# Performance work log

Hardware: AMD Instinct MI355X
Metric: run time of the kernel (lower is better)

## Reference

```python
import jax, jax.numpy as jnp
import numpy as np

B, S, D, H = 2, 2048, 1024, 8
DK = D // H            # 128
TOPK = int(0.25 * S)   # 512, matches int(topk_ratio * attn_scores.shape[-1])


def setup_inputs() -> dict:
    root = jax.random.key(0)
    ks = jax.random.split(root, 11)
    s = 1.0 / np.sqrt(D)  # nn.Linear default init scale
    def lin(kw, kb):
        W = jax.random.uniform(kw, (D, D), jnp.float32, -s, s)
        b = jax.random.uniform(kb, (D,), jnp.float32, -s, s)
        return W, b
    Wq, bq = lin(ks[0], ks[1])
    Wk, bk = lin(ks[2], ks[3])
    Wv, bv = lin(ks[4], ks[5])
    Wo, bo = lin(ks[6], ks[7])
    return {
        "query": jax.random.normal(ks[8], (B, S, D), jnp.float32),
        "key": jax.random.normal(ks[9], (B, S, D), jnp.float32),
        "value": jax.random.normal(ks[10], (B, S, D), jnp.float32),
        "Wq": Wq, "bq": bq, "Wk": Wk, "bk": bk,
        "Wv": Wv, "bv": bv, "Wo": Wo, "bo": bo,
    }


def reference(query, key, value, Wq, bq, Wk, bk, Wv, bv, Wo, bo):
    # Projections + split heads: [B,S,D] -> [B,S,H,DK]
    Q = (query @ Wq + bq).reshape(B, S, H, DK)
    K = (key   @ Wk + bk).reshape(B, S, H, DK)
    V = (value @ Wv + bv).reshape(B, S, H, DK)

    # Full attention scores [B,H,S,S]
    scores = jnp.einsum('nqhd,nkhd->nhqk', Q, K) / np.sqrt(DK).astype(np.float32)

    # Top-k per query row, scatter into a -1e20-filled tensor
    top_val, top_idx = jax.lax.top_k(scores, TOPK)  # [B,H,S,TOPK]
    bi = jnp.arange(B)[:, None, None, None]
    hi = jnp.arange(H)[None, :, None, None]
    qi = jnp.arange(S)[None, None, :, None]
    sparse = jnp.full(scores.shape, -1e20, scores.dtype).at[bi, hi, qi, top_idx].set(top_val)

    weights = jax.nn.softmax(sparse, axis=-1)                      # [B,H,S,S]
    attn = jnp.einsum('nhql,nlhd->nqhd', weights, V).reshape(B, S, D)
    out = attn @ Wo + bo
    return out, weights
```

## Files before the change

kernel.cpp:

```cpp
#include <hip/hip_runtime.h>
#include <hip/hip_bf16.h>
#include <math.h>

namespace {

constexpr int Bb   = 2;
constexpr int Ss   = 2048;
constexpr int Dd   = 1024;
constexpr int Hh   = 8;
constexpr int DKk  = 128;
constexpr int KTOP = 512;
constexpr int BH    = Bb * Hh;
constexpr int MROWS = Bb * Ss;
constexpr float SCALE = 0.08838834764831845f;

typedef __attribute__((ext_vector_type(8))) short short8t;
typedef __attribute__((ext_vector_type(4))) short short4t;
typedef __attribute__((ext_vector_type(4))) float f32x4;

__device__ inline ushort f2bf(float x) {
  const unsigned u = __float_as_uint(x);
  return (ushort)((u + 0x7FFFu + ((u >> 16) & 1u)) >> 16);
}
__device__ inline float bf2f(ushort h) {
  return __uint_as_float(((unsigned)h) << 16);
}
struct HL { short h, l; };
__device__ inline HL split1(float x) {
  HL r;
  const ushort hu = f2bf(x);
  r.h = (short)hu;
  r.l = (short)f2bf(x - bf2f(hu));
  return r;
}

__device__ inline unsigned key_of(float v) {
  const unsigned u = __float_as_uint(v);
  return (u & 0x80000000u) ? ~u : (u | 0x80000000u);
}
__device__ inline float key_to_float(unsigned k) {
  const unsigned u = (k & 0x80000000u) ? (k & 0x7FFFFFFFu) : ~k;
  return __uint_as_float(u);
}

__device__ inline void gload16(const void* g, void* l) {
  __builtin_amdgcn_global_load_lds(
      (const __attribute__((address_space(1))) unsigned int*)g,
      (__attribute__((address_space(3))) unsigned int*)l, 16, 0, 0);
}

__global__ __launch_bounds__(256) void split_inputs(
    const float* __restrict__ query, const float* __restrict__ keyi,
    const float* __restrict__ value,
    ushort* __restrict__ qsh, ushort* __restrict__ qsl,
    ushort* __restrict__ ksh, ushort* __restrict__ ksl,
    ushort* __restrict__ vsb)
{
  const int z = blockIdx.y;
  const size_t i = ((size_t)blockIdx.x * 256 + threadIdx.x) * 8;
  const float* src = (z == 0) ? query : (z == 1) ? keyi : value;
  const float4 v0 = *(const float4*)(src + i);
  const float4 v1 = *(const float4*)(src + i + 4);
  if (z < 2) {
    ushort* oh = (z == 0) ? qsh : ksh;
    ushort* ol = (z == 0) ? qsl : ksl;
    short8t h, lo;
    HL r;
    r = split1(v0.x); h[0] = r.h; lo[0] = r.l;
    r = split1(v0.y); h[1] = r.h; lo[1] = r.l;
    r = split1(v0.z); h[2] = r.h; lo[2] = r.l;
    r = split1(v0.w); h[3] = r.h; lo[3] = r.l;
    r = split1(v1.x); h[4] = r.h; lo[4] = r.l;
    r = split1(v1.y); h[5] = r.h; lo[5] = r.l;
    r = split1(v1.z); h[6] = r.h; lo[6] = r.l;
    r = split1(v1.w); h[7] = r.h; lo[7] = r.l;
    *(short8t*)(oh + i) = h;
    *(short8t*)(ol + i) = lo;
  } else {
    short8t h;
    h[0] = (short)f2bf(v0.x); h[1] = (short)f2bf(v0.y);
    h[2] = (short)f2bf(v0.z); h[3] = (short)f2bf(v0.w);
    h[4] = (short)f2bf(v1.x); h[5] = (short)f2bf(v1.y);
    h[6] = (short)f2bf(v1.z); h[7] = (short)f2bf(v1.w);
    *(short8t*)(vsb + i) = h;
  }
}

__global__ __launch_bounds__(256) void mfma_proj(
    const ushort* __restrict__ qsh, const ushort* __restrict__ qsl,
    const ushort* __restrict__ ksh, const ushort* __restrict__ ksl,
    const ushort* __restrict__ vsb,
    const ushort* __restrict__ WqTh, const ushort* __restrict__ WqTl,
    const ushort* __restrict__ WkTh, const ushort* __restrict__ WkTl,
    const ushort* __restrict__ WvT,
    const float* __restrict__ bq, const float* __restrict__ bk,
    const float* __restrict__ bv,
    ushort* __restrict__ Qh, ushort* __restrict__ Ql,
    ushort* __restrict__ Kh, ushort* __restrict__ Kl,
    ushort* __restrict__ Vt)
{
  __shared__ ushort Ah[128 * 32];
  __shared__ ushort Al[128 * 32];
  __shared__ ushort Bh[128 * 32];
  __shared__ ushort Bl[128 * 32];
  const int t  = threadIdx.x;
  const int z  = blockIdx.z;
  const int m0 = blockIdx.x * 128;
  const int n0 = blockIdx.y * 128;
  const int l  = t & 63, wv = t >> 6;
  const int wr = wv >> 1, wc = wv & 1;
  const int lrow = l & 15, lhi = l >> 4;

  const ushort* Ah_g = (z == 0) ? qsh : (z == 1) ? ksh : vsb;
  const ushort* Al_g = (z == 0) ? qsl : (z == 1) ? ksl : nullptr;
  const ushort* Bth  = (z == 0) ? WqTh : (z == 1) ? WkTh : WvT;
  const ushort* Btl  = (z == 0) ? WqTl : (z == 1) ? WkTl : nullptr;
  const float*  bias = (z == 0) ? bq   : (z == 1) ? bk   : bv;
  const bool    splitTerms = (z < 2);

  f32x4 acc[4][4] = {};

  for (int kt = 0; kt < Dd; kt += 32) {
#pragma unroll
    for (int p = 0; p < 2; ++p) {
      const int baseRow = p * 64 + wv * 16;
      const int row  = baseRow + (l >> 2);
      const int gl   = (l & 3) ^ (row & 3);
      const size_t ao = (size_t)(m0 + row) * Dd + kt + gl * 8;
      const size_t bo = (size_t)(n0 + row) * Dd + kt + gl * 8;
      gload16(Ah_g + ao, &Ah[baseRow * 32]);
      gload16(Bth + bo, &Bh[baseRow * 32]);
      if (splitTerms) {
        gload16(Al_g + ao, &Al[baseRow * 32]);
        gload16(Btl + bo, &Bl[baseRow * 32]);
      }
    }
    __syncthreads();

    short8t ah[4], al[4], bh[4], bl[4];
#pragma unroll
    for (int i = 0; i < 4; ++i) {
      const int row = wr * 64 + i * 16 + lrow;
      const int idx = row * 32 + ((lhi ^ (row & 3)) << 3);
      ah[i] = *(const short8t*)&Ah[idx];
      if (splitTerms) al[i] = *(const short8t*)&Al[idx];
    }
#pragma unroll
    for (int j = 0; j < 4; ++j) {
      const int row = wc * 64 + j * 16 + lrow;
      const int idx = row * 32 + ((lhi ^ (row & 3)) << 3);
      bh[j] = *(const short8t*)&Bh[idx];
      if (splitTerms) bl[j] = *(const short8t*)&Bl[idx];
    }
#pragma unroll
    for (int i = 0; i < 4; ++i)
#pragma unroll
      for (int j = 0; j < 4; ++j) {
        acc[i][j] = __builtin_amdgcn_mfma_f32_16x16x32_bf16(ah[i], bh[j], acc[i][j], 0, 0, 0);
        if (splitTerms) {
          acc[i][j] = __builtin_amdgcn_mfma_f32_16x16x32_bf16(ah[i], bl[j], acc[i][j], 0, 0, 0);
          acc[i][j] = __builtin_amdgcn_mfma_f32_16x16x32_bf16(al[i], bh[j], acc[i][j], 0, 0, 0);
        }
      }
    __syncthreads();
  }

#pragma unroll
  for (int i = 0; i < 4; ++i) {
#pragma unroll
    for (int j = 0; j < 4; ++j) {
      const int nn = n0 + wc * 64 + j * 16 + lrow;
#pragma unroll
      for (int r = 0; r < 4; ++r) {
        const int mm = m0 + wr * 64 + i * 16 + lhi * 4 + r;
        const float v = acc[i][j][r] + bias[nn];
        const int bb = mm >> 11, s = mm & (Ss - 1);
        const int hh = nn >> 7,  dk = nn & (DKk - 1);
        if (z < 2) {
          const size_t o = (((size_t)(bb * Hh + hh)) * Ss + s) * DKk + dk;
          const HL rr = split1(v);
          if (z == 0) { Qh[o] = (ushort)rr.h; Ql[o] = (ushort)rr.l; }
          else        { Kh[o] = (ushort)rr.h; Kl[o] = (ushort)rr.l; }
        } else {
          Vt[((size_t)((bb * Hh + hh) * DKk + dk)) * Ss + s] = f2bf(v);
        }
      }
    }
  }
}

__global__ __launch_bounds__(256) void mfma_scores(
    const ushort* __restrict__ Qh, const ushort* __restrict__ Ql,
    const ushort* __restrict__ Kh, const ushort* __restrict__ Kl,
    unsigned* __restrict__ wtsOut)
{
  __shared__ ushort Ah[128 * 32];
  __shared__ ushort Al[128 * 32];
  __shared__ ushort Bh[128 * 32];
  __shared__ ushort Bl[128 * 32];
  const int t  = threadIdx.x;
  const int z  = blockIdx.z;
  const int n0 = blockIdx.x * 128;
  const int m0 = blockIdx.y * 128;
  const int l  = t & 63, wv = t >> 6;
  const int wr = wv >> 1, wc = wv & 1;
  const int lrow = l & 15, lhi = l >> 4;
  const size_t boff = (size_t)z * Ss * DKk;

  f32x4 acc[4][4] = {};

  for (int kt = 0; kt < DKk; kt += 32) {
#pragma unroll
    for (int p = 0; p < 2; ++p) {
      const int baseRow = p * 64 + wv * 16;
      const int row  = baseRow + (l >> 2);
      const int gl   = (l & 3) ^ (row & 3);
      const size_t ao = boff + (size_t)(m0 + row) * DKk + kt + gl * 8;
      const size_t bo = boff + (size_t)(n0 + row) * DKk + kt + gl * 8;
      gload16(Qh + ao, &Ah[baseRow * 32]);
      gload16(Ql + ao, &Al[baseRow * 32]);
      gload16(Kh + bo, &Bh[baseRow * 32]);
      gload16(Kl + bo, &Bl[baseRow * 32]);
    }
    __syncthreads();

    short8t ah[4], al[4], bh[4], bl[4];
#pragma unroll
    for (int i = 0; i < 4; ++i) {
      const int row = wr * 64 + i * 16 + lrow;
      const int idx = row * 32 + ((lhi ^ (row & 3)) << 3);
      ah[i] = *(const short8t*)&Ah[idx];
      al[i] = *(const short8t*)&Al[idx];
    }
#pragma unroll
    for (int j = 0; j < 4; ++j) {
      const int row = wc * 64 + j * 16 + lrow;
      const int idx = row * 32 + ((lhi ^ (row & 3)) << 3);
      bh[j] = *(const short8t*)&Bh[idx];
      bl[j] = *(const short8t*)&Bl[idx];
    }
#pragma unroll
    for (int i = 0; i < 4; ++i)
#pragma unroll
      for (int j = 0; j < 4; ++j) {
        acc[i][j] = __builtin_amdgcn_mfma_f32_16x16x32_bf16(ah[i], bh[j], acc[i][j], 0, 0, 0);
        acc[i][j] = __builtin_amdgcn_mfma_f32_16x16x32_bf16(ah[i], bl[j], acc[i][j], 0, 0, 0);
        acc[i][j] = __builtin_amdgcn_mfma_f32_16x16x32_bf16(al[i], bh[j], acc[i][j], 0, 0, 0);
      }
    __syncthreads();
  }

#pragma unroll
  for (int i = 0; i < 4; ++i)
#pragma unroll
    for (int j = 0; j < 4; ++j) {
      const int nn = n0 + wc * 64 + j * 16 + lrow;
#pragma unroll
      for (int r = 0; r < 4; ++r) {
        const int mm = m0 + wr * 64 + i * 16 + lhi * 4 + r;
        wtsOut[(size_t)z * Ss * Ss + (size_t)mm * Ss + nn] =
            key_of(acc[i][j][r] * SCALE);
      }
    }
}

__global__ __launch_bounds__(256) void mfma_oproj(
    const float* __restrict__ pv0, const float* __restrict__ pv1,
    const ushort* __restrict__ Bt,
    const float* __restrict__ bias, float* __restrict__ Cout)
{
  __shared__ ushort As[128 * 64];
  __shared__ ushort Bs[128 * 64];
  const int t  = threadIdx.x;
  const int m0 = blockIdx.x * 128;
  const int n0 = blockIdx.y * 128;
  const int l  = t & 63, wv = t >> 6;
  const int wr = wv >> 1, wc = wv & 1;
  const int lrow = l & 15, lhi = l >> 4;

  f32x4 acc[4][4] = {};

  for (int kt = 0; kt < Dd; kt += 64) {
#pragma unroll
    for (int p = 0; p < 4; ++p) {
      const int baseRow = p * 32 + wv * 8;
      const int brow = baseRow + (l >> 3);
      const int bgl  = (l & 7) ^ (brow & 7);
      gload16(Bt + (size_t)(n0 + brow) * Dd + kt + bgl * 8, &Bs[baseRow * 64]);
      const int li = p * 256 + t, row = li >> 3, g = li & 7;
      const int sw = row * 64 + ((g ^ (row & 7)) << 3);
      const size_t ao = (size_t)(m0 + row) * Dd + kt + g * 8;
      const float4 a0 = *(const float4*)(pv0 + ao);
      const float4 a1 = *(const float4*)(pv0 + ao + 4);
      const float4 c0 = *(const float4*)(pv1 + ao);
      const float4 c1 = *(const float4*)(pv1 + ao + 4);
      short8t sa;
      sa[0] = (short)f2bf(a0.x + c0.x); sa[1] = (short)f2bf(a0.y + c0.y);
      sa[2] = (short)f2bf(a0.z + c0.z); sa[3] = (short)f2bf(a0.w + c0.w);
      sa[4] = (short)f2bf(a1.x + c1.x); sa[5] = (short)f2bf(a1.y + c1.y);
      sa[6] = (short)f2bf(a1.z + c1.z); sa[7] = (short)f2bf(a1.w + c1.w);
      *(short8t*)&As[sw] = sa;
    }
    __syncthreads();

#pragma unroll
    for (int kk = 0; kk < 2; ++kk) {
      short8t a[4], b[4];
      const int g = kk * 4 + lhi;
#pragma unroll
      for (int i = 0; i < 4; ++i) {
        const int row = wr * 64 + i * 16 + lrow;
        a[i] = *(const short8t*)&As[row * 64 + ((g ^ (row & 7)) << 3)];
      }
#pragma unroll
      for (int j = 0; j < 4; ++j) {
        const int row = wc * 64 + j * 16 + lrow;
        b[j] = *(const short8t*)&Bs[row * 64 + ((g ^ (row & 7)) << 3)];
      }
#pragma unroll
      for (int i = 0; i < 4; ++i)
#pragma unroll
        for (int j = 0; j < 4; ++j)
          acc[i][j] = __builtin_amdgcn_mfma_f32_16x16x32_bf16(a[i], b[j], acc[i][j], 0, 0, 0);
    }
    __syncthreads();
  }

#pragma unroll
  for (int i = 0; i < 4; ++i)
#pragma unroll
    for (int j = 0; j < 4; ++j) {
      const int nn = n0 + wc * 64 + j * 16 + lrow;
#pragma unroll
      for (int r = 0; r < 4; ++r) {
        const int mm = m0 + wr * 64 + i * 16 + lhi * 4 + r;
        Cout[(size_t)mm * Dd + nn] = acc[i][j][r] + bias[nn];
      }
    }
}

__global__ __launch_bounds__(256) void pv_split(
    const float* __restrict__ Wts, const ushort* __restrict__ VtAll,
    float* __restrict__ pvp)
{
  __shared__ ushort As[128 * 64];
  __shared__ ushort Bs[128 * 64];
  const int t  = threadIdx.x;
  const int ks = blockIdx.x;
  const int m0 = blockIdx.y * 128;
  const int z  = blockIdx.z;
  const int l  = t & 63, wv = t >> 6;
  const int wr = wv >> 1, wc = wv & 1;
  const int lrow = l & 15, lhi = l >> 4;

  const float*  Af = Wts + (size_t)z * Ss * Ss;
  const ushort* Bt = VtAll + (size_t)z * DKk * Ss;

  f32x4 acc[4][4] = {};

  for (int kt = ks * 1024; kt < ks * 1024 + 1024; kt += 64) {
#pragma unroll
    for (int p = 0; p < 4; ++p) {
      const int baseRow = p * 32 + wv * 8;
      const int brow = baseRow + (l >> 3);
      const int bgl  = (l & 7) ^ (brow & 7);
      gload16(Bt + (size_t)brow * Ss + kt + bgl * 8, &Bs[baseRow * 64]);
      const int li = p * 256 + t, row = li >> 3, g = li & 7;
      const int sw = row * 64 + ((g ^ (row & 7)) << 3);
      const float* src = Af + (size_t)(m0 + row) * Ss + kt + g * 8;
      const float4 v0 = *(const float4*)src;
      const float4 v1 = *(const float4*)(src + 4);
      short8t sa;
      sa[0] = (short)f2bf(v0.x); sa[1] = (short)f2bf(v0.y);
      sa[2] = (short)f2bf(v0.z); sa[3] = (short)f2bf(v0.w);
      sa[4] = (short)f2bf(v1.x); sa[5] = (short)f2bf(v1.y);
      sa[6] = (short)f2bf(v1.z); sa[7] = (short)f2bf(v1.w);
      *(short8t*)&As[sw] = sa;
    }
    __syncthreads();

#pragma unroll
    for (int kk = 0; kk < 2; ++kk) {
      short8t a[4], b[4];
      const int g = kk * 4 + lhi;
#pragma unroll
      for (int i = 0; i < 4; ++i) {
        const int row = wr * 64 + i * 16 + lrow;
        a[i] = *(const short8t*)&As[row * 64 + ((g ^ (row & 7)) << 3)];
      }
#pragma unroll
      for (int j = 0; j < 4; ++j) {
        const int row = wc * 64 + j * 16 + lrow;
        b[j] = *(const short8t*)&Bs[row * 64 + ((g ^ (row & 7)) << 3)];
      }
#pragma unroll
      for (int i = 0; i < 4; ++i)
#pragma unroll
        for (int j = 0; j < 4; ++j)
          acc[i][j] = __builtin_amdgcn_mfma_f32_16x16x32_bf16(a[i], b[j], acc[i][j], 0, 0, 0);
    }
    __syncthreads();
  }

  const int bb = z >> 3, hh = z & 7;
  float* outp = pvp + (size_t)ks * MROWS * Dd;
#pragma unroll
  for (int i = 0; i < 4; ++i)
#pragma unroll
    for (int j = 0; j < 4; ++j) {
      const int nn = wc * 64 + j * 16 + lrow;
#pragma unroll
      for (int r = 0; r < 4; ++r) {
        const int mm = m0 + wr * 64 + i * 16 + lhi * 4 + r;
        outp[((size_t)(bb * Ss + mm)) * Dd + hh * DKk + nn] = acc[i][j][r];
      }
    }
}

__global__ __launch_bounds__(256) void transpose_bf16(
    const float* __restrict__ W, ushort* __restrict__ Wt)
{
  __shared__ float tile[32][33];
  const int t  = threadIdx.x;
  const int c0 = blockIdx.x * 32, r0 = blockIdx.y * 32;
  const int lr = t >> 3, lc4 = (t & 7) * 4;
  const float4 v = *(const float4*)(W + (size_t)(r0 + lr) * Dd + c0 + lc4);
  tile[lr][lc4 + 0] = v.x; tile[lr][lc4 + 1] = v.y;
  tile[lr][lc4 + 2] = v.z; tile[lr][lc4 + 3] = v.w;
  __syncthreads();
  const int oc = t >> 3, or4 = (t & 7) * 4;
  short4t o;
  o[0] = (short)f2bf(tile[or4 + 0][oc]);
  o[1] = (short)f2bf(tile[or4 + 1][oc]);
  o[2] = (short)f2bf(tile[or4 + 2][oc]);
  o[3] = (short)f2bf(tile[or4 + 3][oc]);
  *(short4t*)(Wt + (size_t)(c0 + oc) * Dd + r0 + or4) = o;
}

__global__ __launch_bounds__(256) void transpose_split(
    const float* __restrict__ W, ushort* __restrict__ Th, ushort* __restrict__ Tl)
{
  __shared__ float tile[32][33];
  const int t  = threadIdx.x;
  const int c0 = blockIdx.x * 32, r0 = blockIdx.y * 32;
  const int lr = t >> 3, lc4 = (t & 7) * 4;
  const float4 v = *(const float4*)(W + (size_t)(r0 + lr) * Dd + c0 + lc4);
  tile[lr][lc4 + 0] = v.x; tile[lr][lc4 + 1] = v.y;
  tile[lr][lc4 + 2] = v.z; tile[lr][lc4 + 3] = v.w;
  __syncthreads();
  const int oc = t >> 3, or4 = (t & 7) * 4;
  short4t oh, ol;
  HL r;
  r = split1(tile[or4 + 0][oc]); oh[0] = r.h; ol[0] = r.l;
  r = split1(tile[or4 + 1][oc]); oh[1] = r.h; ol[1] = r.l;
  r = split1(tile[or4 + 2][oc]); oh[2] = r.h; ol[2] = r.l;
  r = split1(tile[or4 + 3][oc]); oh[3] = r.h; ol[3] = r.l;
  *(short4t*)(Th + (size_t)(c0 + oc) * Dd + r0 + or4) = oh;
  *(short4t*)(Tl + (size_t)(c0 + oc) * Dd + r0 + or4) = ol;
}

__global__ __launch_bounds__(256) void topk_softmax(float* __restrict__ wts)
{
  __shared__ unsigned histAll[4][1088];

  const int lane = threadIdx.x & 63;
  const int wv   = threadIdx.x >> 6;
  const int row  = blockIdx.x * 4 + wv;
  float* rowp = wts + (size_t)row * Ss;
  unsigned* rowu = (unsigned*)rowp;
  unsigned* h = histAll[wv];

  unsigned k[32];
  unsigned lmax = 0u;
#pragma unroll
  for (int i = 0; i < 8; ++i) {
    const uint4 v = *(const uint4*)(rowu + i * 256 + lane * 4);
    k[i * 4 + 0] = v.x; k[i * 4 + 1] = v.y;
    k[i * 4 + 2] = v.z; k[i * 4 + 3] = v.w;
    lmax = max(max(lmax, max(v.x, v.y)), max(v.z, v.w));
  }
#pragma unroll
  for (int off = 32; off > 0; off >>= 1) lmax = max(lmax, __shfl_xor(lmax, off));
  const float m = key_to_float(lmax);

  unsigned needK = KTOP, tieC = 0u, prefix = 0u;

  {
#pragma unroll
    for (int i = 0; i < 17; ++i) h[lane + i * 64] = 0u;
#pragma unroll
    for (int i = 0; i < 32; ++i) {
      const unsigned b = k[i] >> 22;
      atomicAdd(&h[b + (b >> 4)], 1u);
    }
    unsigned b[16], lsum = 0u;
#pragma unroll
    for (int i = 0; i < 16; ++i) { b[i] = h[lane * 17 + i]; lsum += b[i]; }
    unsigned s = lsum;
#pragma unroll
    for (int off = 1; off < 64; off <<= 1) {
      const unsigned v = __shfl_down(s, off);
      if (lane + off < 64) s += v;
    }
    unsigned run = s - lsum;
    unsigned fb = 0u, fn = 0u, ft = 0u;
    bool found = false;
#pragma unroll
    for (int i = 15; i >= 0; --i) {
      const unsigned c = b[i];
      if (!found && c > 0u && run < needK && run + c >= needK) {
        found = true; fb = (unsigned)(lane * 16 + i); fn = needK - run; ft = c;
      }
      run += c;
    }
    const unsigned long long msk = __ballot(found);
    const int src = (int)__ffsll(msk) - 1;
    prefix = __shfl(fb, src) << 22;
    needK  = __shfl(fn, src);
    tieC   = __shfl(ft, src);
  }

#pragma unroll
  for (int pass = 0; pass < 2; ++pass) {
    const int sh = (pass == 0) ? 14 : 6;
    const int ph = sh + 8;
#pragma unroll
    for (int i = 0; i < 5; ++i) h[lane + i * 64] = 0u;
    const unsigned pcmp = prefix >> ph;
#pragma unroll
    for (int i = 0; i < 32; ++i) {
      if ((k[i] >> ph) == pcmp) {
        const unsigned b = (k[i] >> sh) & 255u;
        atomicAdd(&h[b + (b >> 4)], 1u);
      }
    }
    unsigned b4[4], lsum = 0u;
#pragma unroll
    for (int i = 0; i < 4; ++i) {
      const unsigned x = (unsigned)(lane * 4 + i);
      b4[i] = h[x + (x >> 4)];
      lsum += b4[i];
    }
    unsigned s = lsum;
#pragma unroll
    for (int off = 1; off < 64; off <<= 1) {
      const unsigned v = __shfl_down(s, off);
      if (lane + off < 64) s += v;
    }
    unsigned run = s - lsum;
    unsigned fb = 0u, fn = 0u, ft = 0u;
    bool found = false;
#pragma unroll
    for (int i = 3; i >= 0; --i) {
      const unsigned c = b4[i];
      if (!found && c > 0u && run < needK && run + c >= needK) {
        found = true; fb = (unsigned)(lane * 4 + i); fn = needK - run; ft = c;
      }
      run += c;
    }
    const unsigned long long msk = __ballot(found);
    const int src = (int)__ffsll(msk) - 1;
    prefix |= __shfl(fb, src) << sh;
    needK   = __shfl(fn, src);
    tieC    = __shfl(ft, src);
  }

  unsigned T;
  {
    h[lane] = 0u;
    if (lane < 4) h[64 + lane] = 0u;
    const unsigned pcmp = prefix >> 6;
#pragma unroll
    for (int i = 0; i < 32; ++i) {
      if ((k[i] >> 6) == pcmp) {
        const unsigned b = k[i] & 63u;
        atomicAdd(&h[b + (b >> 4)], 1u);
      }
    }
    const unsigned b0 = h[lane + (lane >> 4)];
    unsigned s = b0;
#pragma unroll
    for (int off = 1; off < 64; off <<= 1) {
      const unsigned v = __shfl_down(s, off);
      if (lane + off < 64) s += v;
    }
    const unsigned run = s - b0;
    const bool found = (b0 > 0u && run < needK && run + b0 >= needK);
    const unsigned long long msk = __ballot(found);
    const int src = (int)__ffsll(msk) - 1;
    T     = prefix | (unsigned)__shfl((unsigned)lane, src);
    needK = __shfl(needK - run, src);
    tieC  = __shfl(b0, src);
  }

  if (tieC != needK) {
    unsigned R = 0u;
#pragma unroll
    for (int i = 0; i < 8; ++i) {
      unsigned myEq = 0u;
#pragma unroll
      for (int c = 0; c < 4; ++c) myEq += (k[i * 4 + c] == T);
      unsigned ps = myEq;
#pragma unroll
      for (int off = 1; off < 64; off <<= 1) {
        const unsigned v = __shfl_up(ps, off);
        if (lane >= off) ps += v;
      }
      unsigned before = R + ps - myEq;
#pragma unroll
      for (int c = 0; c < 4; ++c) {
        if (k[i * 4 + c] == T) {
          if (before >= needK) k[i * 4 + c] = 0u;
          ++before;
        }
      }
      R += __shfl(ps, 63);
    }
  }

  float lz = 0.f;
#pragma unroll
  for (int i = 0; i < 32; ++i) {
    const unsigned kk = k[i];
    const float w = (kk >= T) ? __expf(key_to_float(kk) - m) : 0.f;
    k[i] = __float_as_uint(w);
    lz += w;
  }
#pragma unroll
  for (int off = 32; off > 0; off >>= 1) lz += __shfl_xor(lz, off);
  const float Zi = 1.0f / lz;

#pragma unroll
  for (int i = 0; i < 8; ++i) {
    float4 o;
    o.x = __uint_as_float(k[i * 4 + 0]) * Zi;
    o.y = __uint_as_float(k[i * 4 + 1]) * Zi;
    o.z = __uint_as_float(k[i * 4 + 2]) * Zi;
    o.w = __uint_as_float(k[i * 4 + 3]) * Zi;
    *(float4*)(rowu + i * 256 + lane * 4) = o;
  }
}

}

extern "C" void kernel_launch(void* const* d_in, const int* in_sizes, int n_in,
                              void* d_out_v, int out_size, void* d_ws, size_t ws_size,
                              hipStream_t stream)
{
  const float* query = (const float*)d_in[0];
  const float* key   = (const float*)d_in[1];
  const float* value = (const float*)d_in[2];
  const float* Wq = (const float*)d_in[3];  const float* bq = (const float*)d_in[4];
  const float* Wk = (const float*)d_in[5];  const float* bk = (const float*)d_in[6];
  const float* Wv = (const float*)d_in[7];  const float* bv = (const float*)d_in[8];
  const float* Wo = (const float*)d_in[9];  const float* bo = (const float*)d_in[10];

  float* d_out = (float*)d_out_v;
  float* outp  = d_out;
  float* wts   = d_out + (size_t)Bb * Ss * Dd;

  const size_t PROJ = (size_t)MROWS * Dd;
  const size_t DD2  = (size_t)Dd * Dd;

  ushort* ws    = (ushort*)d_ws;
  ushort* Qh    = ws;
  ushort* Ql    = Qh + PROJ;
  ushort* Kh    = Ql + PROJ;
  ushort* Kl    = Kh + PROJ;
  ushort* wreg  = Kl + PROJ;
  ushort* WqTh  = wreg;
  ushort* WqTl  = wreg + DD2;
  ushort* WkTh  = wreg + 2 * DD2;
  ushort* WkTl  = wreg + 3 * DD2;
  ushort* WvT   = wreg + 4 * DD2;
  ushort* WoT   = wreg + 5 * DD2;
  ushort* Vt    = wreg + 6 * DD2;
  float*  pvp   = (float*)Qh;

  ushort* qsh = (ushort*)wts;
  ushort* qsl = qsh + PROJ;
  ushort* ksh = qsh + 2 * PROJ;
  ushort* ksl = qsh + 3 * PROJ;
  ushort* vsb = qsh + 4 * PROJ;

  const dim3 blk(256);

  transpose_split<<<dim3(32, 32), blk, 0, stream>>>(Wq, WqTh, WqTl);
  transpose_split<<<dim3(32, 32), blk, 0, stream>>>(Wk, WkTh, WkTl);
  transpose_bf16<<<dim3(32, 32), blk, 0, stream>>>(Wv, WvT);
  transpose_bf16<<<dim3(32, 32), blk, 0, stream>>>(Wo, WoT);

  split_inputs<<<dim3((int)(PROJ / 2048), 3), blk, 0, stream>>>(
      query, key, value, qsh, qsl, ksh, ksl, vsb);

  mfma_proj<<<dim3(MROWS / 128, Dd / 128, 3), blk, 0, stream>>>(
      qsh, qsl, ksh, ksl, vsb, WqTh, WqTl, WkTh, WkTl, WvT,
      bq, bk, bv, Qh, Ql, Kh, Kl, Vt);

  mfma_scores<<<dim3(Ss / 128, Ss / 128, BH), blk, 0, stream>>>(
      Qh, Ql, Kh, Kl, (unsigned*)wts);

  topk_softmax<<<dim3(BH * Ss / 4), blk, 0, stream>>>(wts);

  pv_split<<<dim3(2, Ss / 128, BH), blk, 0, stream>>>(wts, Vt, pvp);

  mfma_oproj<<<dim3(MROWS / 128, Dd / 128), blk, 0, stream>>>(
      pvp, pvp + (size_t)MROWS * Dd, WoT, bo, outp);
}
```

Before: 387.1 us.

## Fuse top-k softmax with PV matmul and merge weight transposes

Merges the top-k/softmax kernel with the probability-times-V product. Each block handles 16 query rows, normalizes them, then immediately multiplies them against V with MFMA, reducing across four waves in shared memory and writing bf16 attention output. This drops the split-K fp32 partial buffers and the separate re-read of the weights tile. The output projection now loads bf16 directly, and the four weight-transpose launches are combined into one. The risks are that PV now reads A and V straight from global memory without LDS tiling, and that V is re-read by every 16-row block.

```diff
diff --git a/kernel.cpp b/kernel.cpp
--- a/kernel.cpp
+++ b/kernel.cpp
@@ -86,6 +86,47 @@
   }
 }
 
+__global__ __launch_bounds__(256) void transpose_prep(
+    const float* __restrict__ Wq, const float* __restrict__ Wk,
+    const float* __restrict__ Wv, const float* __restrict__ Wo,
+    ushort* __restrict__ WqTh, ushort* __restrict__ WqTl,
+    ushort* __restrict__ WkTh, ushort* __restrict__ WkTl,
+    ushort* __restrict__ WvT,  ushort* __restrict__ WoT)
+{
+  __shared__ float tile[32][33];
+  const int z = blockIdx.z;
+  const float* W = (z == 0) ? Wq : (z == 1) ? Wk : (z == 2) ? Wv : Wo;
+  const int t  = threadIdx.x;
+  const int c0 = blockIdx.x * 32, r0 = blockIdx.y * 32;
+  const int lr = t >> 3, lc4 = (t & 7) * 4;
+  const float4 v = *(const float4*)(W + (size_t)(r0 + lr) * Dd + c0 + lc4);
+  tile[lr][lc4 + 0] = v.x; tile[lr][lc4 + 1] = v.y;
+  tile[lr][lc4 + 2] = v.z; tile[lr][lc4 + 3] = v.w;
+  __syncthreads();
+  const int oc = t >> 3, or4 = (t & 7) * 4;
+  const size_t o = (size_t)(c0 + oc) * Dd + r0 + or4;
+  if (z < 2) {
+    ushort* Th = (z == 0) ? WqTh : WkTh;
+    ushort* Tl = (z == 0) ? WqTl : WkTl;
+    short4t oh, ol;
+    HL r;
+    r = split1(tile[or4 + 0][oc]); oh[0] = r.h; ol[0] = r.l;
+    r = split1(tile[or4 + 1][oc]); oh[1] = r.h; ol[1] = r.l;
+    r = split1(tile[or4 + 2][oc]); oh[2] = r.h; ol[2] = r.l;
+    r = split1(tile[or4 + 3][oc]); oh[3] = r.h; ol[3] = r.l;
+    *(short4t*)(Th + o) = oh;
+    *(short4t*)(Tl + o) = ol;
+  } else {
+    ushort* Wt = (z == 2) ? WvT : WoT;
+    short4t ov;
+    ov[0] = (short)f2bf(tile[or4 + 0][oc]);
+    ov[1] = (short)f2bf(tile[or4 + 1][oc]);
+    ov[2] = (short)f2bf(tile[or4 + 2][oc]);
+    ov[3] = (short)f2bf(tile[or4 + 3][oc]);
+    *(short4t*)(Wt + o) = ov;
+  }
+}
+
 __global__ __launch_bounds__(256) void mfma_proj(
     const ushort* __restrict__ qsh, const ushort* __restrict__ qsl,
     const ushort* __restrict__ ksh, const ushort* __restrict__ ksl,
@@ -264,9 +305,262 @@
     }
 }
 
+__global__ __launch_bounds__(256) void topk_pv(
+    float* __restrict__ wts, const ushort* __restrict__ VtAll,
+    ushort* __restrict__ attnb)
+{
+  __shared__ unsigned histAll[4][1088];
+  __shared__ float    red[2][16][128];
+
+  const int t    = threadIdx.x;
+  const int lane = t & 63;
+  const int wv   = t >> 6;
+  const int bh   = blockIdx.x >> 7;
+  const int q0   = (blockIdx.x & 127) * 16;
+  unsigned* h = histAll[wv];
+
+  for (int rr = 0; rr < 4; ++rr) {
+    const int row = q0 + wv * 4 + rr;
+    float* rowp = wts + ((size_t)bh * Ss + row) * Ss;
+    unsigned* rowu = (unsigned*)rowp;
+
+    unsigned k[32];
+    unsigned lmax = 0u;
+#pragma unroll
+    for (int i = 0; i < 8; ++i) {
+      const uint4 v = *(const uint4*)(rowu + i * 256 + lane * 4);
+      k[i * 4 + 0] = v.x; k[i * 4 + 1] = v.y;
+      k[i * 4 + 2] = v.z; k[i * 4 + 3] = v.w;
+      lmax = max(max(lmax, max(v.x, v.y)), max(v.z, v.w));
+    }
+#pragma unroll
+    for (int off = 32; off > 0; off >>= 1) lmax = max(lmax, __shfl_xor(lmax, off));
+    const float m = key_to_float(lmax);
+
+    unsigned needK = KTOP, tieC = 0u, prefix = 0u;
+
+    {
+#pragma unroll
+      for (int i = 0; i < 17; ++i) h[lane + i * 64] = 0u;
+#pragma unroll
+      for (int i = 0; i < 32; ++i) {
+        const unsigned b = k[i] >> 22;
+        atomicAdd(&h[b + (b >> 4)], 1u);
+      }
+      unsigned b[16], lsum = 0u;
+#pragma unroll
+      for (int i = 0; i < 16; ++i) { b[i] = h[lane * 17 + i]; lsum += b[i]; }
+      unsigned s = lsum;
+#pragma unroll
+      for (int off = 1; off < 64; off <<= 1) {
+        const unsigned v = __shfl_down(s, off);
+        if (lane + off < 64) s += v;
+      }
+      unsigned run = s - lsum;
+      unsigned fb = 0u, fn = 0u, ft = 0u;
+      bool found = false;
+#pragma unroll
+      for (int i = 15; i >= 0; --i) {
+        const unsigned c = b[i];
+        if (!found && c > 0u && run < needK && run + c >= needK) {
+          found = true; fb = (unsigned)(lane * 16 + i); fn = needK - run; ft = c;
+        }
+        run += c;
+      }
+      const unsigned long long msk = __ballot(found);
+      const int src = (int)__ffsll(msk) - 1;
+      prefix = __shfl(fb, src) << 22;
+      needK  = __shfl(fn, src);
+      tieC   = __shfl(ft, src);
+    }
+
+#pragma unroll
+    for (int pass = 0; pass < 2; ++pass) {
+      const int sh = (pass == 0) ? 14 : 6;
+      const int ph = sh + 8;
+#pragma unroll
+      for (int i = 0; i < 5; ++i) h[lane + i * 64] = 0u;
+      const unsigned pcmp = prefix >> ph;
+#pragma unroll
+      for (int i = 0; i < 32; ++i) {
+        if ((k[i] >> ph) == pcmp) {
+          const unsigned b = (k[i] >> sh) & 255u;
+          atomicAdd(&h[b + (b >> 4)], 1u);
+        }
+      }
+      unsigned b4[4], lsum = 0u;
+#pragma unroll
+      for (int i = 0; i < 4; ++i) {
+        const unsigned x = (unsigned)(lane * 4 + i);
+        b4[i] = h[x + (x >> 4)];
+        lsum += b4[i];
+      }
+      unsigned s = lsum;
+#pragma unroll
+      for (int off = 1; off < 64; off <<= 1) {
+        const unsigned v = __shfl_down(s, off);
+        if (lane + off < 64) s += v;
+      }
+      unsigned run = s - lsum;
+      unsigned fb = 0u, fn = 0u, ft = 0u;
+      bool found = false;
+#pragma unroll
+      for (int i = 3; i >= 0; --i) {
+        const unsigned c = b4[i];
+        if (!found && c > 0u && run < needK && run + c >= needK) {
+          found = true; fb = (unsigned)(lane * 4 + i); fn = needK - run; ft = c;
+        }
+        run += c;
+      }
+      const unsigned long long msk = __ballot(found);
+      const int src = (int)__ffsll(msk) - 1;
+      prefix |= __shfl(fb, src) << sh;
+      needK   = __shfl(fn, src);
+      tieC    = __shfl(ft, src);
+    }
+
+    unsigned T;
+    {
+      h[lane] = 0u;
+      if (lane < 4) h[64 + lane] = 0u;
+      const unsigned pcmp = prefix >> 6;
+#pragma unroll
+      for (int i = 0; i < 32; ++i) {
+        if ((k[i] >> 6) == pcmp) {
+          const unsigned b = k[i] & 63u;
+          atomicAdd(&h[b + (b >> 4)], 1u);
+        }
+      }
+      const unsigned b0 = h[lane + (lane >> 4)];
+      unsigned s = b0;
+#pragma unroll
+      for (int off = 1; off < 64; off <<= 1) {
+        const unsigned v = __shfl_down(s, off);
+        if (lane + off < 64) s += v;
+      }
+      const unsigned run = s - b0;
+      const bool found = (b0 > 0u && run < needK && run + b0 >= needK);
+      const unsigned long long msk = __ballot(found);
+      const int src = (int)__ffsll(msk) - 1;
+      T     = prefix | (unsigned)__shfl((unsigned)lane, src);
+      needK = __shfl(needK - run, src);
+      tieC  = __shfl(b0, src);
+    }
+
+    if (tieC != needK) {
+      unsigned R = 0u;
+#pragma unroll
+      for (int i = 0; i < 8; ++i) {
+        unsigned myEq = 0u;
+#pragma unroll
+        for (int c = 0; c < 4; ++c) myEq += (k[i * 4 + c] == T);
+        unsigned ps = myEq;
+#pragma unroll
+        for (int off = 1; off < 64; off <<= 1) {
+          const unsigned v = __shfl_up(ps, off);
+          if (lane >= off) ps += v;
+        }
+        unsigned before = R + ps - myEq;
+#pragma unroll
+        for (int c = 0; c < 4; ++c) {
+          if (k[i * 4 + c] == T) {
+            if (before >= needK) k[i * 4 + c] = 0u;
+            ++before;
+          }
+        }
+        R += __shfl(ps, 63);
+      }
+    }
+
+    float lz = 0.f;
+#pragma unroll
+    for (int i = 0; i < 32; ++i) {
+      const unsigned kk = k[i];
+      const float w = (kk >= T) ? __expf(key_to_float(kk) - m) : 0.f;
+      k[i] = __float_as_uint(w);
+      lz += w;
+    }
+#pragma unroll
+    for (int off = 32; off > 0; off >>= 1) lz += __shfl_xor(lz, off);
+    const float Zi = 1.0f / lz;
+
+#pragma unroll
+    for (int i = 0; i < 8; ++i) {
+      float4 o;
+      o.x = __uint_as_float(k[i * 4 + 0]) * Zi;
+      o.y = __uint_as_float(k[i * 4 + 1]) * Zi;
+      o.z = __uint_as_float(k[i * 4 + 2]) * Zi;
+      o.w = __uint_as_float(k[i * 4 + 3]) * Zi;
+      *(float4*)(rowu + i * 256 + lane * 4) = o;
+    }
+  }
+
+  __syncthreads();
+
+  const float*  wrow0 = wts + ((size_t)bh * Ss + q0) * Ss;
+  const ushort* Vt    = VtAll + (size_t)bh * DKk * Ss;
+  const int lrow = lane & 15, lhi = lane >> 4;
+
+  f32x4 acc[8] = {};
+  const int j0base = wv * 512;
+  for (int ks = 0; ks < 16; ++ks) {
+    const int j0 = j0base + ks * 32;
+    const float* ap = wrow0 + (size_t)lrow * Ss + j0 + lhi * 8;
+    const float4 a0 = *(const float4*)ap;
+    const float4 a1 = *(const float4*)(ap + 4);
+    short8t af;
+    af[0] = (short)f2bf(a0.x); af[1] = (short)f2bf(a0.y);
+    af[2] = (short)f2bf(a0.z); af[3] = (short)f2bf(a0.w);
+    af[4] = (short)f2bf(a1.x); af[5] = (short)f2bf(a1.y);
+    af[6] = (short)f2bf(a1.z); af[7] = (short)f2bf(a1.w);
+#pragma unroll
+    for (int jt = 0; jt < 8; ++jt) {
+      const short8t bf_ = *(const short8t*)(
+          Vt + (size_t)(jt * 16 + lrow) * Ss + j0 + lhi * 8);
+      acc[jt] = __builtin_amdgcn_mfma_f32_16x16x32_bf16(af, bf_, acc[jt], 0, 0, 0);
+    }
+  }
+
+  if (wv >= 2) {
+#pragma unroll
+    for (int jt = 0; jt < 8; ++jt)
+#pragma unroll
+      for (int r = 0; r < 4; ++r)
+        red[wv - 2][lhi * 4 + r][jt * 16 + lrow] = acc[jt][r];
+  }
+  __syncthreads();
+  if (wv < 2) {
+#pragma unroll
+    for (int jt = 0; jt < 8; ++jt)
+#pragma unroll
+      for (int r = 0; r < 4; ++r)
+        acc[jt][r] += red[wv][lhi * 4 + r][jt * 16 + lrow];
+  }
+  __syncthreads();
+  if (wv == 1) {
+#pragma unroll
+    for (int jt = 0; jt < 8; ++jt)
+#pragma unroll
+      for (int r = 0; r < 4; ++r)
+        red[0][lhi * 4 + r][jt * 16 + lrow] = acc[jt][r];
+  }
+  __syncthreads();
+  if (wv == 0) {
+    const int bb = bh >> 3, hh = bh & 7;
+#pragma unroll
+    for (int jt = 0; jt < 8; ++jt)
+#pragma unroll
+      for (int r = 0; r < 4; ++r) {
+        const int row = lhi * 4 + r;
+        const int dk  = jt * 16 + lrow;
+        const float v = acc[jt][r] + red[0][row][dk];
+        attnb[((size_t)(bb * Ss + q0 + row)) * Dd + hh * DKk + dk] = f2bf(v);
+      }
+  }
+}
+
 __global__ __launch_bounds__(256) void mfma_oproj(
-    const float* __restrict__ pv0, const float* __restrict__ pv1,
-    const ushort* __restrict__ Bt,
+    const ushort* __restrict__ Ab, const ushort* __restrict__ Bt,
     const float* __restrict__ bias, float* __restrict__ Cout)
 {
   __shared__ ushort As[128 * 64];
@@ -284,22 +578,10 @@
 #pragma unroll
     for (int p = 0; p < 4; ++p) {
       const int baseRow = p * 32 + wv * 8;
-      const int brow = baseRow + (l >> 3);
-      const int bgl  = (l & 7) ^ (brow & 7);
-      gload16(Bt + (size_t)(n0 + brow) * Dd + kt + bgl * 8, &Bs[baseRow * 64]);
-      const int li = p * 256 + t, row = li >> 3, g = li & 7;
-      const int sw = row * 64 + ((g ^ (row & 7)) << 3);
-      const size_t ao = (size_t)(m0 + row) * Dd + kt + g * 8;
-      const float4 a0 = *(const float4*)(pv0 + ao);
-      const float4 a1 = *(const float4*)(pv0 + ao + 4);
-      const float4 c0 = *(const float4*)(pv1 + ao);
-      const float4 c1 = *(const float4*)(pv1 + ao + 4);
-      short8t sa;
-      sa[0] = (short)f2bf(a0.x + c0.x); sa[1] = (short)f2bf(a0.y + c0.y);
-      sa[2] = (short)f2bf(a0.z + c0.z); sa[3] = (short)f2bf(a0.w + c0.w);
-      sa[4] = (short)f2bf(a1.x + c1.x); sa[5] = (short)f2bf(a1.y + c1.y);
-      sa[6] = (short)f2bf(a1.z + c1.z); sa[7] = (short)f2bf(a1.w + c1.w);
-      *(short8t*)&As[sw] = sa;
+      const int row = baseRow + (l >> 3);
+      const int gl  = (l & 7) ^ (row & 7);
+      gload16(Ab + (size_t)(m0 + row) * Dd + kt + gl * 8, &As[baseRow * 64]);
+      gload16(Bt + (size_t)(n0 + row) * Dd + kt + gl * 8, &Bs[baseRow * 64]);
     }
     __syncthreads();
 
@@ -337,308 +619,6 @@
         Cout[(size_t)mm * Dd + nn] = acc[i][j][r] + bias[nn];
       }
     }
-}
-
-__global__ __launch_bounds__(256) void pv_split(
-    const float* __restrict__ Wts, const ushort* __restrict__ VtAll,
-    float* __restrict__ pvp)
-{
-  __shared__ ushort As[128 * 64];
-  __shared__ ushort Bs[128 * 64];
-  const int t  = threadIdx.x;
-  const int ks = blockIdx.x;
-  const int m0 = blockIdx.y * 128;
-  const int z  = blockIdx.z;
-  const int l  = t & 63, wv = t >> 6;
-  const int wr = wv >> 1, wc = wv & 1;
-  const int lrow = l & 15, lhi = l >> 4;
-
-  const float*  Af = Wts + (size_t)z * Ss * Ss;
-  const ushort* Bt = VtAll + (size_t)z * DKk * Ss;
-
-  f32x4 acc[4][4] = {};
-
-  for (int kt = ks * 1024; kt < ks * 1024 + 1024; kt += 64) {
-#pragma unroll
-    for (int p = 0; p < 4; ++p) {
-      const int baseRow = p * 32 + wv * 8;
-      const int brow = baseRow + (l >> 3);
-      const int bgl  = (l & 7) ^ (brow & 7);
-      gload16(Bt + (size_t)brow * Ss + kt + bgl * 8, &Bs[baseRow * 64]);
-      const int li = p * 256 + t, row = li >> 3, g = li & 7;
-      const int sw = row * 64 + ((g ^ (row & 7)) << 3);
-      const float* src = Af + (size_t)(m0 + row) * Ss + kt + g * 8;
-      const float4 v0 = *(const float4*)src;
-      const float4 v1 = *(const float4*)(src + 4);
-      short8t sa;
-      sa[0] = (short)f2bf(v0.x); sa[1] = (short)f2bf(v0.y);
-      sa[2] = (short)f2bf(v0.z); sa[3] = (short)f2bf(v0.w);
-      sa[4] = (short)f2bf(v1.x); sa[5] = (short)f2bf(v1.y);
-      sa[6] = (short)f2bf(v1.z); sa[7] = (short)f2bf(v1.w);
-      *(short8t*)&As[sw] = sa;
-    }
-    __syncthreads();
-
-#pragma unroll
-    for (int kk = 0; kk < 2; ++kk) {
-      short8t a[4], b[4];
-      const int g = kk * 4 + lhi;
-#pragma unroll
-      for (int i = 0; i < 4; ++i) {
-        const int row = wr * 64 + i * 16 + lrow;
-        a[i] = *(const short8t*)&As[row * 64 + ((g ^ (row & 7)) << 3)];
-      }
-#pragma unroll
-      for (int j = 0; j < 4; ++j) {
-        const int row = wc * 64 + j * 16 + lrow;
-        b[j] = *(const short8t*)&Bs[row * 64 + ((g ^ (row & 7)) << 3)];
-      }
-#pragma unroll
-      for (int i = 0; i < 4; ++i)
-#pragma unroll
-        for (int j = 0; j < 4; ++j)
-          acc[i][j] = __builtin_amdgcn_mfma_f32_16x16x32_bf16(a[i], b[j], acc[i][j], 0, 0, 0);
-    }
-    __syncthreads();
-  }
-
-  const int bb = z >> 3, hh = z & 7;
-  float* outp = pvp + (size_t)ks * MROWS * Dd;
-#pragma unroll
-  for (int i = 0; i < 4; ++i)
-#pragma unroll
-    for (int j = 0; j < 4; ++j) {
-      const int nn = wc * 64 + j * 16 + lrow;
-#pragma unroll
-      for (int r = 0; r < 4; ++r) {
-        const int mm = m0 + wr * 64 + i * 16 + lhi * 4 + r;
-        outp[((size_t)(bb * Ss + mm)) * Dd + hh * DKk + nn] = acc[i][j][r];
-      }
-    }
-}
-
-__global__ __launch_bounds__(256) void transpose_bf16(
-    const float* __restrict__ W, ushort* __restrict__ Wt)
-{
-  __shared__ float tile[32][33];
-  const int t  = threadIdx.x;
-  const int c0 = blockIdx.x * 32, r0 = blockIdx.y * 32;
-  const int lr = t >> 3, lc4 = (t & 7) * 4;
-  const float4 v = *(const float4*)(W + (size_t)(r0 + lr) * Dd + c0 + lc4);
-  tile[lr][lc4 + 0] = v.x; tile[lr][lc4 + 1] = v.y;
-  tile[lr][lc4 + 2] = v.z; tile[lr][lc4 + 3] = v.w;
-  __syncthreads();
-  const int oc = t >> 3, or4 = (t & 7) * 4;
-  short4t o;
-  o[0] = (short)f2bf(tile[or4 + 0][oc]);
-  o[1] = (short)f2bf(tile[or4 + 1][oc]);
-  o[2] = (short)f2bf(tile[or4 + 2][oc]);
-  o[3] = (short)f2bf(tile[or4 + 3][oc]);
-  *(short4t*)(Wt + (size_t)(c0 + oc) * Dd + r0 + or4) = o;
-}
-
-__global__ __launch_bounds__(256) void transpose_split(
-    const float* __restrict__ W, ushort* __restrict__ Th, ushort* __restrict__ Tl)
-{
-  __shared__ float tile[32][33];
-  const int t  = threadIdx.x;
-  const int c0 = blockIdx.x * 32, r0 = blockIdx.y * 32;
-  const int lr = t >> 3, lc4 = (t & 7) * 4;
-  const float4 v = *(const float4*)(W + (size_t)(r0 + lr) * Dd + c0 + lc4);
-  tile[lr][lc4 + 0] = v.x; tile[lr][lc4 + 1] = v.y;
-  tile[lr][lc4 + 2] = v.z; tile[lr][lc4 + 3] = v.w;
-  __syncthreads();
-  const int oc = t >> 3, or4 = (t & 7) * 4;
-  short4t oh, ol;
-  HL r;
-  r = split1(tile[or4 + 0][oc]); oh[0] = r.h; ol[0] = r.l;
-  r = split1(tile[or4 + 1][oc]); oh[1] = r.h; ol[1] = r.l;
-  r = split1(tile[or4 + 2][oc]); oh[2] = r.h; ol[2] = r.l;
-  r = split1(tile[or4 + 3][oc]); oh[3] = r.h; ol[3] = r.l;
-  *(short4t*)(Th + (size_t)(c0 + oc) * Dd + r0 + or4) = oh;
-  *(short4t*)(Tl + (size_t)(c0 + oc) * Dd + r0 + or4) = ol;
-}
-
-__global__ __launch_bounds__(256) void topk_softmax(float* __restrict__ wts)
-{
-  __shared__ unsigned histAll[4][1088];
-
-  const int lane = threadIdx.x & 63;
-  const int wv   = threadIdx.x >> 6;
-  const int row  = blockIdx.x * 4 + wv;
-  float* rowp = wts + (size_t)row * Ss;
-  unsigned* rowu = (unsigned*)rowp;
-  unsigned* h = histAll[wv];
-
-  unsigned k[32];
-  unsigned lmax = 0u;
-#pragma unroll
-  for (int i = 0; i < 8; ++i) {
-    const uint4 v = *(const uint4*)(rowu + i * 256 + lane * 4);
-    k[i * 4 + 0] = v.x; k[i * 4 + 1] = v.y;
-    k[i * 4 + 2] = v.z; k[i * 4 + 3] = v.w;
-    lmax = max(max(lmax, max(v.x, v.y)), max(v.z, v.w));
-  }
-#pragma unroll
-  for (int off = 32; off > 0; off >>= 1) lmax = max(lmax, __shfl_xor(lmax, off));
-  const float m = key_to_float(lmax);
-
-  unsigned needK = KTOP, tieC = 0u, prefix = 0u;
-
-  {
-#pragma unroll
-    for (int i = 0; i < 17; ++i) h[lane + i * 64] = 0u;
-#pragma unroll
-    for (int i = 0; i < 32; ++i) {
-      const unsigned b = k[i] >> 22;
-      atomicAdd(&h[b + (b >> 4)], 1u);
-    }
-    unsigned b[16], lsum = 0u;
-#pragma unroll
-    for (int i = 0; i < 16; ++i) { b[i] = h[lane * 17 + i]; lsum += b[i]; }
-    unsigned s = lsum;
-#pragma unroll
-    for (int off = 1; off < 64; off <<= 1) {
-      const unsigned v = __shfl_down(s, off);
-      if (lane + off < 64) s += v;
-    }
-    unsigned run = s - lsum;
-    unsigned fb = 0u, fn = 0u, ft = 0u;
-    bool found = false;
-#pragma unroll
-    for (int i = 15; i >= 0; --i) {
-      const unsigned c = b[i];
-      if (!found && c > 0u && run < needK && run + c >= needK) {
-        found = true; fb = (unsigned)(lane * 16 + i); fn = needK - run; ft = c;
-      }
-      run += c;
-    }
-    const unsigned long long msk = __ballot(found);
-    const int src = (int)__ffsll(msk) - 1;
-    prefix = __shfl(fb, src) << 22;
-    needK  = __shfl(fn, src);
-    tieC   = __shfl(ft, src);
-  }
-
-#pragma unroll
-  for (int pass = 0; pass < 2; ++pass) {
-    const int sh = (pass == 0) ? 14 : 6;
-    const int ph = sh + 8;
-#pragma unroll
-    for (int i = 0; i < 5; ++i) h[lane + i * 64] = 0u;
-    const unsigned pcmp = prefix >> ph;
-#pragma unroll
-    for (int i = 0; i < 32; ++i) {
-      if ((k[i] >> ph) == pcmp) {
-        const unsigned b = (k[i] >> sh) & 255u;
-        atomicAdd(&h[b + (b >> 4)], 1u);
-      }
-    }
-    unsigned b4[4], lsum = 0u;
-#pragma unroll
-    for (int i = 0; i < 4; ++i) {
-      const unsigned x = (unsigned)(lane * 4 + i);
-      b4[i] = h[x + (x >> 4)];
-      lsum += b4[i];
-    }
-    unsigned s = lsum;
-#pragma unroll
-    for (int off = 1; off < 64; off <<= 1) {
-      const unsigned v = __shfl_down(s, off);
-      if (lane + off < 64) s += v;
-    }
-    unsigned run = s - lsum;
-    unsigned fb = 0u, fn = 0u, ft = 0u;
-    bool found = false;
-#pragma unroll
-    for (int i = 3; i >= 0; --i) {
-      const unsigned c = b4[i];
-      if (!found && c > 0u && run < needK && run + c >= needK) {
-        found = true; fb = (unsigned)(lane * 4 + i); fn = needK - run; ft = c;
-      }
-      run += c;
-    }
-    const unsigned long long msk = __ballot(found);
-    const int src = (int)__ffsll(msk) - 1;
-    prefix |= __shfl(fb, src) << sh;
-    needK   = __shfl(fn, src);
-    tieC    = __shfl(ft, src);
-  }
-
-  unsigned T;
-  {
-    h[lane] = 0u;
-    if (lane < 4) h[64 + lane] = 0u;
-    const unsigned pcmp = prefix >> 6;
-#pragma unroll
-    for (int i = 0; i < 32; ++i) {
-      if ((k[i] >> 6) == pcmp) {
-        const unsigned b = k[i] & 63u;
-        atomicAdd(&h[b + (b >> 4)], 1u);
-      }
-    }
-    const unsigned b0 = h[lane + (lane >> 4)];
-    unsigned s = b0;
-#pragma unroll
-    for (int off = 1; off < 64; off <<= 1) {
-      const unsigned v = __shfl_down(s, off);
-      if (lane + off < 64) s += v;
-    }
-    const unsigned run = s - b0;
-    const bool found = (b0 > 0u && run < needK && run + b0 >= needK);
-    const unsigned long long msk = __ballot(found);
-    const int src = (int)__ffsll(msk) - 1;
-    T     = prefix | (unsigned)__shfl((unsigned)lane, src);
-    needK = __shfl(needK - run, src);
-    tieC  = __shfl(b0, src);
-  }
-
-  if (tieC != needK) {
-    unsigned R = 0u;
-#pragma unroll
-    for (int i = 0; i < 8; ++i) {
-      unsigned myEq = 0u;
-#pragma unroll
-      for (int c = 0; c < 4; ++c) myEq += (k[i * 4 + c] == T);
-      unsigned ps = myEq;
-#pragma unroll
-      for (int off = 1; off < 64; off <<= 1) {
-        const unsigned v = __shfl_up(ps, off);
-        if (lane >= off) ps += v;
-      }
-      unsigned before = R + ps - myEq;
-#pragma unroll
-      for (int c = 0; c < 4; ++c) {
-        if (k[i * 4 + c] == T) {
-          if (before >= needK) k[i * 4 + c] = 0u;
-          ++before;
-        }
-      }
-      R += __shfl(ps, 63);
-    }
-  }
-
-  float lz = 0.f;
-#pragma unroll
-  for (int i = 0; i < 32; ++i) {
-    const unsigned kk = k[i];
-    const float w = (kk >= T) ? __expf(key_to_float(kk) - m) : 0.f;
-    k[i] = __float_as_uint(w);
-    lz += w;
-  }
-#pragma unroll
-  for (int off = 32; off > 0; off >>= 1) lz += __shfl_xor(lz, off);
-  const float Zi = 1.0f / lz;
-
-#pragma unroll
-  for (int i = 0; i < 8; ++i) {
-    float4 o;
-    o.x = __uint_as_float(k[i * 4 + 0]) * Zi;
-    o.y = __uint_as_float(k[i * 4 + 1]) * Zi;
-    o.z = __uint_as_float(k[i * 4 + 2]) * Zi;
-    o.w = __uint_as_float(k[i * 4 + 3]) * Zi;
-    *(float4*)(rowu + i * 256 + lane * 4) = o;
-  }
 }
 
 }
@@ -675,7 +655,7 @@
   ushort* WvT   = wreg + 4 * DD2;
   ushort* WoT   = wreg + 5 * DD2;
   ushort* Vt    = wreg + 6 * DD2;
-  float*  pvp   = (float*)Qh;
+  ushort* attnb = Qh;
 
   ushort* qsh = (ushort*)wts;
   ushort* qsl = qsh + PROJ;
@@ -685,10 +665,8 @@
 
   const dim3 blk(256);
 
-  transpose_split<<<dim3(32, 32), blk, 0, stream>>>(Wq, WqTh, WqTl);
-  transpose_split<<<dim3(32, 32), blk, 0, stream>>>(Wk, WkTh, WkTl);
-  transpose_bf16<<<dim3(32, 32), blk, 0, stream>>>(Wv, WvT);
-  transpose_bf16<<<dim3(32, 32), blk, 0, stream>>>(Wo, WoT);
+  transpose_prep<<<dim3(32, 32, 4), blk, 0, stream>>>(
+      Wq, Wk, Wv, Wo, WqTh, WqTl, WkTh, WkTl, WvT, WoT);
 
   split_inputs<<<dim3((int)(PROJ / 2048), 3), blk, 0, stream>>>(
       query, key, value, qsh, qsl, ksh, ksl, vsb);
@@ -700,10 +678,8 @@
   mfma_scores<<<dim3(Ss / 128, Ss / 128, BH), blk, 0, stream>>>(
       Qh, Ql, Kh, Kl, (unsigned*)wts);
 
-  topk_softmax<<<dim3(BH * Ss / 4), blk, 0, stream>>>(wts);
-
-  pv_split<<<dim3(2, Ss / 128, BH), blk, 0, stream>>>(wts, Vt, pvp);
+  topk_pv<<<dim3(BH * Ss / 16), blk, 0, stream>>>(wts, Vt, attnb);
 
   mfma_oproj<<<dim3(MROWS / 128, Dd / 128), blk, 0, stream>>>(
-      pvp, pvp + (size_t)MROWS * Dd, WoT, bo, outp);
-}
+      attnb, WoT, bo, outp);
+}
```

Result: slower. 456.3 us (+17.9%).
